# Optimization experiments

Measured on AMD Instinct MI355X. Metric: run time of the kernel, lower is better.

Reference implementation:

```python
import jax, jax.numpy as jnp
import numpy as np

N_RNA, N_DIS = 40000, 3000
E_EDGES, T = 600000, 10000
RNA_IN, D_FEAT, HID, EXP_D = 512, 256, 512, 256
N_EXP, HEADS = 8, 8
HD = HID // HEADS          # per-head dim inside HANConv
MHA_HD = EXP_D // HEADS    # per-head dim in cross-attention
FUSION = 2 * HID


def setup_inputs() -> dict:
    key = jax.random.key(0)
    ks = iter(jax.random.split(key, 48))
    def nrm(shape, s=0.02):
        return jax.random.normal(next(ks), shape, dtype=jnp.float32) * s
    inp = {
        "x_rna": jax.random.normal(next(ks), (N_RNA, RNA_IN), dtype=jnp.float32),
        "x_dis": jax.random.normal(next(ks), (N_DIS, D_FEAT), dtype=jnp.float32),
        "Wd": nrm((RNA_IN, D_FEAT)), "bd": jnp.zeros((RNA_IN,), jnp.float32),
        "Wp_r": nrm((HID, RNA_IN)), "bp_r": jnp.zeros((HID,), jnp.float32),
        "Wp_d": nrm((HID, RNA_IN)), "bp_d": jnp.zeros((HID,), jnp.float32),
        "a_src_rd": nrm((HEADS, HD), 0.1), "a_dst_rd": nrm((HEADS, HD), 0.1),
        "a_src_dr": nrm((HEADS, HD), 0.1), "a_dst_dr": nrm((HEADS, HD), 0.1),
        "kW": nrm((HID, HID)), "kb": jnp.zeros((HID,), jnp.float32),
        "qv": nrm((HID,), 0.1),
        "Wl": nrm((HID, HID)), "bl": jnp.zeros((HID,), jnp.float32),
        "W_exp": nrm((N_EXP, FUSION, EXP_D)), "b_exp": jnp.zeros((N_EXP, EXP_D), jnp.float32),
        "W_gate": nrm((4, HID, N_EXP)),
        "W_head": nrm((4, 2 * EXP_D, EXP_D)), "b_head": jnp.zeros((4, EXP_D), jnp.float32),
        "in_w": nrm((3 * EXP_D, EXP_D)), "in_b": jnp.zeros((3 * EXP_D,), jnp.float32),
        "out_w": nrm((EXP_D, EXP_D)), "out_b": jnp.zeros((EXP_D,), jnp.float32),
        "Wdp": nrm((EXP_D, HID)), "bdp": jnp.zeros((EXP_D,), jnp.float32),
        "ei_rd_src": jax.random.randint(next(ks), (E_EDGES,), 0, N_RNA),
        "ei_rd_dst": jax.random.randint(next(ks), (E_EDGES,), 0, N_DIS),
        "ei_dr_src": jax.random.randint(next(ks), (E_EDGES,), 0, N_DIS),
        "ei_dr_dst": jax.random.randint(next(ks), (E_EDGES,), 0, N_RNA),
        "idx_rels": jax.random.randint(next(ks), (4, T), 0, N_RNA),
    }
    return inp


def _han_edge(x_src, x_dst, ei_src, ei_dst, a_src, a_dst, n_dst):
    # x_*: [N, H, D]; GAT-style attention with softmax per destination node (PyG HANConv edge step)
    as_ = (x_src * a_src).sum(-1)                                 # [Ns, H]
    ad_ = (x_dst * a_dst).sum(-1)                                 # [Nd, H]
    alpha = jax.nn.leaky_relu(as_[ei_src] + ad_[ei_dst], 0.2)     # [E, H]
    amax = jax.ops.segment_max(alpha, ei_dst, num_segments=n_dst)
    ex = jnp.exp(alpha - amax[ei_dst])
    den = jax.ops.segment_sum(ex, ei_dst, num_segments=n_dst)
    w = ex / (den[ei_dst] + 1e-16)
    msg = x_src[ei_src] * w[:, :, None]                           # [E, H, D]
    out = jax.ops.segment_sum(msg, ei_dst, num_segments=n_dst)    # [Nd, H, D]
    return jax.nn.relu(out.reshape(n_dst, -1))


def _semantic(outs, kW, kb, qv):
    # outs: [M, N, F]; metapath-level (semantic) attention from HANConv
    s = (jnp.tanh(outs @ kW.T + kb).mean(axis=1) * qv).sum(-1)    # [M]
    beta = jax.nn.softmax(s)
    return (beta[:, None, None] * outs).sum(0)


def reference(x_rna, x_dis, Wd, bd, Wp_r, bp_r, Wp_d, bp_d,
              a_src_rd, a_dst_rd, a_src_dr, a_dst_dr,
              kW, kb, qv, Wl, bl, W_exp, b_exp, W_gate, W_head, b_head,
              in_w, in_b, out_w, out_b, Wdp, bdp,
              ei_rd_src, ei_rd_dst, ei_dr_src, ei_dr_dst, idx_rels):
    # ---- HAN encoder ----
    xd = x_dis @ Wd.T + bd                                        # disease feat -> rna_in_dim
    hr0 = (x_rna @ Wp_r.T + bp_r).reshape(N_RNA, HEADS, HD)
    hd0 = (xd @ Wp_d.T + bp_d).reshape(N_DIS, HEADS, HD)
    out_dis = _han_edge(hr0, hd0, ei_rd_src, ei_rd_dst, a_src_rd, a_dst_rd, N_DIS)
    out_rna = _han_edge(hd0, hr0, ei_dr_src, ei_dr_dst, a_src_dr, a_dst_dr, N_RNA)
    h_rna = _semantic(out_rna[None], kW, kb, qv) @ Wl.T + bl      # shared final lin
    h_dis = _semantic(out_dis[None], kW, kb, qv) @ Wl.T + bl
    # ---- MoE with per-relation gating ----
    d_global = h_dis.mean(axis=0)
    fusion = jnp.concatenate([h_rna, jnp.broadcast_to(d_global, h_rna.shape)], axis=1)  # [N, 2H]
    E = jax.nn.relu(jnp.einsum('nf,efd->ned', fusion, W_exp) + b_exp)  # [N, Nexp, Ed]
    h_t = h_rna[idx_rels]                                         # [4, T, H]
    scores = jnp.einsum('rth,rhe->rte', h_t, W_gate)              # raw gate scores (no softmax)
    u = (E[idx_rels] * scores[..., None]).sum(axis=2)             # [4, T, Ed]
    U = u.mean(axis=1)                                            # [4, Ed]
    # ---- cross attention over 4 task tokens ----
    qkv = U @ in_w.T + in_b
    q, k, v = jnp.split(qkv, 3, axis=-1)
    def heads(z):
        return z.reshape(4, HEADS, MHA_HD).transpose(1, 0, 2)     # [H, 4, dh]
    qh, kh, vh = heads(q), heads(k), heads(v)
    attn = jax.nn.softmax(jnp.einsum('htd,hsd->hts', qh, kh) / np.float32(np.sqrt(MHA_HD)), axis=-1)
    o = jnp.einsum('hts,hsd->htd', attn, vh).transpose(1, 0, 2).reshape(4, EXP_D)
    U_prime = o @ out_w.T + out_b                                 # [4, Ed]
    # ---- per-relation heads and disease scores ----
    cross = jnp.broadcast_to(U_prime[:, None, :], u.shape)
    cat = jnp.concatenate([u, cross], axis=-1)                    # [4, T, 2Ed]
    p = jax.nn.relu(jnp.einsum('rtc,rcd->rtd', cat, W_head) + b_head[:, None, :])
    d_proj = h_dis @ Wdp.T + bdp                                  # [Ndis, Ed]
    return jax.nn.sigmoid(jnp.einsum('rtd,md->rtm', p, d_proj))   # [4, T, Ndis]
```

## Files before the change

kernel.cpp:

```cpp
#include <hip/hip_runtime.h>
#include <math.h>

constexpr int NRNA = 40000;
constexpr int NDIS = 3000;
constexpr int NEDG = 600000;
constexpr int TREL = 10000;

typedef __attribute__((ext_vector_type(8))) short bh8;
typedef __attribute__((ext_vector_type(4))) float f32x4;

__device__ inline float bf2f(ushort x) {
    union { uint u; float f; } v; v.u = ((uint)x) << 16; return v.f;
}
__device__ inline ushort f2bf(float f) {
    union { float f; uint u; } v; v.f = f;
    uint u = v.u;
    uint r = (u + 0x7fffu + ((u >> 16) & 1u)) >> 16;
    return (ushort)r;
}
__device__ inline float bflo(uint w) { union { uint u; float f; } v; v.u = w << 16; return v.f; }
__device__ inline float bfhi(uint w) { union { uint u; float f; } v; v.u = w & 0xffff0000u; return v.f; }

__device__ inline void gload16(const ushort* g, ushort* l) {
    __builtin_amdgcn_global_load_lds(
        (const __attribute__((address_space(1))) unsigned int*)(const void*)g,
        (__attribute__((address_space(3))) unsigned int*)(void*)l, 16, 0, 0);
}

__device__ inline int xcd_swz(int f, int n) {
    int q = n >> 3, r = n & 7, xcd = f & 7, i = f >> 3;
    return (xcd < r) ? (xcd * (q + 1) + i) : (r * (q + 1) + (xcd - r) * q + i);
}

__global__ __launch_bounds__(256) void conv_bf16(const float* __restrict__ in,
                                                 ushort* __restrict__ out, long n)
{
    long g = ((long)blockIdx.x * 256 + threadIdx.x) * 4;
    if (g >= n) return;
    float4 v = *(const float4*)(in + g);
    ushort4 o;
    o.x = f2bf(v.x); o.y = f2bf(v.y); o.z = f2bf(v.z); o.w = f2bf(v.w);
    *(ushort4*)(out + g) = o;
}

__global__ __launch_bounds__(256) void transpose_wexp(const float* __restrict__ W,
                                                      ushort* __restrict__ out)
{
    long g = (long)blockIdx.x * 256 + threadIdx.x;
    int e = (int)(g >> 17), d = (int)((g >> 9) & 255), f = (int)(g & 511);
    out[g] = f2bf(W[(long)e * 262144 + (long)f * 256 + d]);
}

__global__ __launch_bounds__(256) void transpose_whead(const float* __restrict__ W,
                                                       ushort* __restrict__ out)
{
    long g = (long)blockIdx.x * 256 + threadIdx.x;
    int r = (int)(g >> 16), d = (int)((g >> 8) & 255), c = (int)(g & 255);
    out[g] = f2bf(W[(long)r * 131072 + (long)c * 256 + d]);
}

__global__ void transpose_wgate(const float* __restrict__ W, float* __restrict__ out)
{
    int g = blockIdx.x * 256 + threadIdx.x;
    int r = g >> 12, e = (g >> 9) & 7, k = g & 511;
    out[g] = W[(long)r * 4096 + (long)k * 8 + e];
}

template<int ACT, bool SWZ>
__global__ __launch_bounds__(256) void gemm_mfma(
    const ushort* __restrict__ A, const ushort* __restrict__ B,
    const float* __restrict__ bias, float* __restrict__ Cf, ushort* __restrict__ Cb,
    const int* __restrict__ idx,
    int M, int N, int K, long sA, long sB, long sBias, long sC)
{
    __shared__ ushort smem[16384];
    ushort* As = smem;
    ushort* Bs = smem + 8192;
    int bx = blockIdx.x, by = blockIdx.y;
    if (SWZ) {
        int n = gridDim.x * gridDim.y;
        int s = xcd_swz(by * gridDim.x + bx, n);
        bx = s % gridDim.x; by = s / gridDim.x;
    }
    const int bz = blockIdx.z;
    const ushort* Ab = A + (long)bz * sA;
    const ushort* Bb = B + (long)bz * sB;
    const float* biasb = bias ? (bias + (long)bz * sBias) : nullptr;
    const int row0 = by * 128, col0 = bx * 128;

    const int tid = threadIdx.x, wid = tid >> 6, lane = tid & 63;
    const int wr = wid >> 1, wc = wid & 1;

    const int lrow = lane >> 3;
    const int lk = (((lane & 7) ^ lrow) * 8);
    const ushort* ap0[4]; const ushort* bp0[4];
    ushort* la[4]; ushort* lb[4];
#pragma unroll
    for (int i = 0; i < 4; ++i) {
        int c = wid * 4 + i;
        int ra = row0 + c * 8 + lrow; ra = ra < M ? ra : M - 1;
        int rs = idx ? idx[ra] : ra;
        ap0[i] = Ab + (long)rs * K + lk;
        int cb = col0 + c * 8 + lrow; cb = cb < N ? cb : N - 1;
        bp0[i] = Bb + (long)cb * K + lk;
        la[i] = As + c * 512;
        lb[i] = Bs + c * 512;
    }

    f32x4 acc[4][4];
#pragma unroll
    for (int i = 0; i < 4; ++i)
// ... 45 lines not shown
        for (int it = 0; it < 8; ++it) {
            int rl = it * 16 + (tid >> 4);
            int cl = (tid & 15) * 4;
            int m = row0 + rl, col = col0 + H * 64 + cl;
            if (m < M && col < N) {
                f32x4 v = *(const f32x4*)(cs + rl * 64 + cl);
                if (biasb) {
                    float4 bv = *(const float4*)(biasb + col);
                    v[0] += bv.x; v[1] += bv.y; v[2] += bv.z; v[3] += bv.w;
                }
                if (ACT == 1) {
#pragma unroll
                    for (int q = 0; q < 4; ++q) v[q] = fmaxf(v[q], 0.f);
                } else if (ACT == 2) {
#pragma unroll
                    for (int q = 0; q < 4; ++q) v[q] = 1.f / (1.f + __expf(-v[q]));
                }
                long o = (long)bz * sC + (long)m * N + col;
                if (Cf) *(f32x4*)(Cf + o) = v;
                if (Cb) {
                    ushort4 ob;
                    ob.x = f2bf(v[0]); ob.y = f2bf(v[1]); ob.z = f2bf(v[2]); ob.w = f2bf(v[3]);
                    *(ushort4*)(Cb + o) = ob;
                }
            }
        }
        __syncthreads();
    }
}

__global__ __launch_bounds__(256) void moe_mfma(
    const ushort* __restrict__ h, const ushort* __restrict__ WexpT,
    const float* __restrict__ c_exp, const float* __restrict__ S,
    const int* __restrict__ idx, ushort* __restrict__ up)
{
    __shared__ ushort smem[24576];
    __shared__ float sS[128 * 2];
    __shared__ float sC[2 * 128];
    ushort* As  = smem;
    ushort* Bs0 = smem + 8192;
    ushort* Bs1 = smem + 16384;
    int bx = blockIdx.x, by = blockIdx.y;
    {
        int n = gridDim.x * gridDim.y;
        int s = xcd_swz(by * gridDim.x + bx, n);
        bx = s % gridDim.x; by = s / gridDim.x;
    }
    const int row0 = by * 128, col0 = bx * 128;
    const int z = blockIdx.z, e0 = z * 2;
    const int tid = threadIdx.x, wid = tid >> 6, lane = tid & 63;
    const int wr = wid >> 1, wc = wid & 1;
    constexpr int M = 4 * TREL;

    if (tid < 256) {
        int rr = tid >> 1, e = tid & 1;
        sS[tid] = S[(long)(row0 + rr) * 8 + e0 + e];
    }
    if (tid < 256) {
        int e = tid >> 7, cc = tid & 127;
        sC[tid] = c_exp[(e0 + e) * 256 + col0 + cc];
    }

    const int lrow = lane >> 3;
    const int lk = (((lane & 7) ^ lrow) * 8);
    const ushort* ap0[4]; const ushort* bp0[4];
    ushort* la[4]; ushort* lb0[4]; ushort* lb1[4];
#pragma unroll
    for (int i = 0; i < 4; ++i) {
        int c = wid * 4 + i;
        int ra = row0 + c * 8 + lrow;
        ap0[i] = h + (long)idx[ra] * 512 + lk;
        bp0[i] = WexpT + (long)(col0 + c * 8 + lrow) * 512 + (long)e0 * 131072 + lk;
        la[i]  = As  + c * 512;
        lb0[i] = Bs0 + c * 512;
        lb1[i] = Bs1 + c * 512;
    }

    const int fr = lane & 15, fq = lane >> 4;
    const int sw0 = (fq ^ (fr & 7)) * 8;
    const ushort* paRow  = As  + (wr * 64 + fr) * 64;
    const ushort* pb0Row = Bs0 + (wc * 64 + fr) * 64;
    const ushort* pb1Row = Bs1 + (wc * 64 + fr) * 64;

    f32x4 acc0[4][4], acc1[4][4];
#pragma unroll
    for (int i = 0; i < 4; ++i)
#pragma unroll
        for (int n = 0; n < 4; ++n) {
            acc0[i][n] = (f32x4){0.f, 0.f, 0.f, 0.f};
            acc1[i][n] = (f32x4){0.f, 0.f, 0.f, 0.f};
        }
    __syncthreads();

    for (int k0 = 0; k0 < 512; k0 += 64) {
#pragma unroll
        for (int i = 0; i < 4; ++i) gload16(ap0[i] + k0, la[i]);
#pragma unroll
        for (int i = 0; i < 4; ++i) gload16(bp0[i] + k0, lb0[i]);
#pragma unroll
        for (int i = 0; i < 4; ++i) gload16(bp0[i] + 131072 + k0, lb1[i]);
        __syncthreads();
#pragma unroll
        for (int kk = 0; kk < 2; ++kk) {
            const int sw = kk ? (sw0 ^ 32) : sw0;
            bh8 af[4], b0[4], b1[4];
#pragma unroll
            for (int i = 0; i < 4; ++i) af[i] = *(const bh8*)(paRow + i * 1024 + sw);
#pragma unroll
            for (int n = 0; n < 4; ++n) b0[n] = *(const bh8*)(pb0Row + n * 1024 + sw);
#pragma unroll
            for (int n = 0; n < 4; ++n) b1[n] = *(const bh8*)(pb1Row + n * 1024 + sw);
#pragma unroll
            for (int i = 0; i < 4; ++i)
// ... 18 lines not shown
                float s0 = sS[(rl + r) * 2 + 0];
                float s1 = sS[(rl + r) * 2 + 1];
                acc0[i][n][r] = s0 * fmaxf(acc0[i][n][r] + c0, 0.f)
                              + s1 * fmaxf(acc1[i][n][r] + c1, 0.f);
            }
        }
    }

    float* cs = (float*)smem;
    ushort* upz = up + (long)z * M * 256;
#pragma unroll
    for (int H = 0; H < 2; ++H) {
        if (wc == H) {
#pragma unroll
            for (int i = 0; i < 4; ++i)
#pragma unroll
                for (int n = 0; n < 4; ++n)
#pragma unroll
                    for (int r = 0; r < 4; ++r)
                        cs[(wr * 64 + i * 16 + fq * 4 + r) * 64 + n * 16 + fr] = acc0[i][n][r];
        }
        __syncthreads();
#pragma unroll
        for (int it = 0; it < 8; ++it) {
            int rl = it * 16 + (tid >> 4);
            int cl = (tid & 15) * 4;
            f32x4 v = *(const f32x4*)(cs + rl * 64 + cl);
            int m = row0 + rl, col = col0 + H * 64 + cl;
            ushort4 ob;
            ob.x = f2bf(v[0]); ob.y = f2bf(v[1]); ob.z = f2bf(v[2]); ob.w = f2bf(v[3]);
            *(ushort4*)(upz + (long)m * 256 + col) = ob;
        }
        __syncthreads();
    }
}

__global__ __launch_bounds__(256) void moe_combine(const ushort* __restrict__ up,
                                                   ushort* __restrict__ u)
{
    constexpr long TOT = (long)4 * TREL * 256;
    long g = ((long)blockIdx.x * 256 + threadIdx.x) * 4;
    if (g >= TOT) return;
    float a[4] = {0.f, 0.f, 0.f, 0.f};
#pragma unroll
    for (int z = 0; z < 4; ++z) {
        ushort4 v = *(const ushort4*)(up + z * TOT + g);
        a[0] += bf2f(v.x); a[1] += bf2f(v.y); a[2] += bf2f(v.z); a[3] += bf2f(v.w);
    }
    ushort4 o;
    o.x = f2bf(a[0]); o.y = f2bf(a[1]); o.z = f2bf(a[2]); o.w = f2bf(a[3]);
    *(ushort4*)(u + g) = o;
}

__global__ void dot_heads2(const ushort* __restrict__ x,
                           const float* __restrict__ a1, const float* __restrict__ a2,
                           float* __restrict__ o1, float* __restrict__ o2, int nodes)
{
    long g = (long)blockIdx.x * 256 + threadIdx.x;
    if (g >= (long)nodes * 8) return;
    int node = (int)(g >> 3), h = (int)(g & 7);
    const ushort* xp = x + (long)node * 512 + h * 64;
    const float* p1 = a1 + h * 64;
    const float* p2 = a2 + h * 64;
    float s1 = 0.f, s2 = 0.f;
#pragma unroll
    for (int d = 0; d < 64; d += 8) {
        uint4 xv = *(const uint4*)(xp + d);
        float xf[8] = { bflo(xv.x), bfhi(xv.x), bflo(xv.y), bfhi(xv.y),
                        bflo(xv.z), bfhi(xv.z), bflo(xv.w), bfhi(xv.w) };
#pragma unroll
        for (int j = 0; j < 8; ++j) {
            s1 = fmaf(xf[j], p1[d + j], s1);
            s2 = fmaf(xf[j], p2[d + j], s2);
        }
    }
    o1[g] = s1; o2[g] = s2;
}

__global__ void hist_kernel(const int* __restrict__ dst, int* __restrict__ deg, int E)
{
    int g = blockIdx.x * 256 + threadIdx.x;
    if (g < E) atomicAdd(&deg[dst[g]], 1);
}

__global__ __launch_bounds__(1024) void scan_blocks(const int* __restrict__ in,
                                                    int* __restrict__ tmp,
                                                    int* __restrict__ bsum, int n)
{
    __shared__ int wsum[16];
    const int tid = threadIdx.x, lane = tid & 63, wid = tid >> 6;
    int base = blockIdx.x * 1024;
    int v = (base + tid < n) ? in[base + tid] : 0;
    int s = v;
#pragma unroll
    for (int off = 1; off < 64; off <<= 1) {
        int t = __shfl_up(s, off, 64);
        if (lane >= off) s += t;
    }
    if (lane == 63) wsum[wid] = s;
    __syncthreads();
    if (wid == 0) {
        int w = (lane < 16) ? wsum[lane] : 0;
#pragma unroll
        for (int off = 1; off < 16; off <<= 1) {
            int t = __shfl_up(w, off, 64);
            if (lane >= off) w += t;
        }
        if (lane < 16) wsum[lane] = w;
    }
    __syncthreads();
    int incl = s + ((wid == 0) ? 0 : wsum[wid - 1]);
    if (base + tid < n) tmp[base + tid] = incl;
    if (tid == 1023) bsum[blockIdx.x] = incl;
}

__global__ void scan_bsums(int* __restrict__ bsum, int nb)
{
    int lane = threadIdx.x;
    int v = (lane < nb) ? bsum[lane] : 0;
#pragma unroll
    for (int off = 1; off < 64; off <<= 1) {
        int t = __shfl_up(v, off, 64);
        if (lane >= off) v += t;
    }
    if (lane < nb) bsum[lane] = v;
}

__global__ __launch_bounds__(1024) void scan_finish(const int* __restrict__ in,
                                                    const int* __restrict__ tmp,
                                                    const int* __restrict__ bsum,
                                                    int* __restrict__ offs,
                                                    int* __restrict__ cur, int n, int nb)
{
    int base = blockIdx.x * 1024;
    int i = base + threadIdx.x;
    if (i < n) {
        int pre = (blockIdx.x == 0) ? 0 : bsum[blockIdx.x - 1];
        int v = tmp[i] - in[i] + pre;
        offs[i] = v;
        cur[i] = v;
    }
    if (i == 0) offs[n] = bsum[nb - 1];
}

__global__ void scatter_kernel(const int* __restrict__ src, const int* __restrict__ dst,
                               int* __restrict__ cur, int* __restrict__ csr_src, int E)
{
    int g = blockIdx.x * 256 + threadIdx.x;
    if (g < E) {
        int p = atomicAdd(&cur[dst[g]], 1);
        csr_src[p] = src[g];
    }
}

__global__ __launch_bounds__(256) void han_wave(
    const int* __restrict__ offs, const int* __restrict__ csr_src,
    const float* __restrict__ as_, const float* __restrict__ ad_,
    const ushort* __restrict__ x_src, ushort* __restrict__ out, int nnode)
{
    __shared__ float s_ex[4][64];
    __shared__ int   s_src[4][8];
    __shared__ float s_den[4][8];
    const int w = threadIdx.x >> 6, lane = threadIdx.x & 63;
    const int node = blockIdx.x * 4 + w;
    if (node >= nnode) return;
    const int e0 = offs[node], ne = offs[node + 1] - e0;
    const int myh = lane & 7, grp = lane >> 3;
    const float my_ad = ad_[node * 8 + myh];

    float mx = -3.0e38f;
    for (int t = grp; t < ne; t += 8) {
        int src = csr_src[e0 + t];
        float al = as_[(long)src * 8 + myh] + my_ad;
        al = al >= 0.f ? al : 0.2f * al;
        mx = fmaxf(mx, al);
    }
#pragma unroll
    for (int m = 8; m < 64; m <<= 1) mx = fmaxf(mx, __shfl_xor(mx, m, 64));

    float den = 0.f;
    float acc[8];
#pragma unroll
    for (int k = 0; k < 8; ++k) acc[k] = 0.f;
    const int colbase = lane * 8;

    for (int c0 = 0; c0 < ne; c0 += 8) {
        const int nc = min(8, ne - c0);
        float ex = 0.f;
        int src = 0;
        if (grp < nc) {
            src = csr_src[e0 + c0 + grp];
            float al = as_[(long)src * 8 + myh] + my_ad;
            al = al >= 0.f ? al : 0.2f * al;
            ex = __expf(al - mx);
            den += ex;
        }
        s_ex[w][grp * 8 + myh] = ex;
        if (myh == 0) s_src[w][grp] = src;
        asm volatile("s_waitcnt lgkmcnt(0)" ::: "memory");
        for (int j = 0; j < nc; ++j) {
            float wg = s_ex[w][j * 8 + grp];
            uint4 xv = *(const uint4*)(x_src + (long)s_src[w][j] * 512 + colbase);
            acc[0] = fmaf(wg, bflo(xv.x), acc[0]);
            acc[1] = fmaf(wg, bfhi(xv.x), acc[1]);
            acc[2] = fmaf(wg, bflo(xv.y), acc[2]);
            acc[3] = fmaf(wg, bfhi(xv.y), acc[3]);
            acc[4] = fmaf(wg, bflo(xv.z), acc[4]);
            acc[5] = fmaf(wg, bfhi(xv.z), acc[5]);
            acc[6] = fmaf(wg, bflo(xv.w), acc[6]);
            acc[7] = fmaf(wg, bfhi(xv.w), acc[7]);
        }
        __builtin_amdgcn_wave_barrier();
    }

#pragma unroll
    for (int m = 8; m < 64; m <<= 1) den += __shfl_xor(den, m, 64);
    if (grp == 0) s_den[w][myh] = den;
    asm volatile("s_waitcnt lgkmcnt(0)" ::: "memory");
    float d = s_den[w][grp] + 1e-16f;

    uint4 ov;
    ov.x = (uint)f2bf(fmaxf(acc[0] / d, 0.f)) | ((uint)f2bf(fmaxf(acc[1] / d, 0.f)) << 16);
    ov.y = (uint)f2bf(fmaxf(acc[2] / d, 0.f)) | ((uint)f2bf(fmaxf(acc[3] / d, 0.f)) << 16);
    ov.z = (uint)f2bf(fmaxf(acc[4] / d, 0.f)) | ((uint)f2bf(fmaxf(acc[5] / d, 0.f)) << 16);
    ov.w = (uint)f2bf(fmaxf(acc[6] / d, 0.f)) | ((uint)f2bf(fmaxf(acc[7] / d, 0.f)) << 16);
    *(uint4*)(out + (long)node * 512 + colbase) = ov;
}

__global__ __launch_bounds__(512) void hdis_colsum_partial(const float* __restrict__ h_dis,
                                                           float* __restrict__ part)
{
    int c = blockIdx.x, d = threadIdx.x;
    int r0 = c * 200;
    float s = 0.f;
    for (int r = r0; r < r0 + 200; ++r) s += h_dis[(long)r * 512 + d];
    part[c * 512 + d] = s;
}
__global__ __launch_bounds__(512) void hdis_colsum_finish(const float* __restrict__ part,
                                                          float* __restrict__ dg)
{
    int d = threadIdx.x;
    float s = 0.f;
    for (int c = 0; c < 15; ++c) s += part[c * 512 + d];
    dg[d] = s * (1.f / NDIS);
}

__global__ void cexp_part(const float* __restrict__ dg, const float* __restrict__ W_exp,
                          float* __restrict__ part)
{
    int b = blockIdx.x;
    int e = b >> 3, ch = b & 7, d = threadIdx.x;
    const float* W = W_exp + (long)e * 262144 + (long)(512 + ch * 64) * 256 + d;
    float s = 0.f;
    for (int f = 0; f < 64; ++f) s = fmaf(dg[ch * 64 + f], W[(long)f * 256], s);
    part[b * 256 + d] = s;
}
__global__ void cexp_fin(const float* __restrict__ part, const float* __restrict__ b_exp,
                         float* __restrict__ c_exp)
{
    int e = blockIdx.x, d = threadIdx.x;
    float s = b_exp[e * 256 + d];
    for (int ch = 0; ch < 8; ++ch) s += part[(e * 8 + ch) * 256 + d];
    c_exp[e * 256 + d] = s;
}

__global__ __launch_bounds__(256) void scores2(const ushort* __restrict__ h,
                                               const float* __restrict__ WgT,
                                               const int* __restrict__ idx,
                                               float* __restrict__ S)
{
    __shared__ float sW[8 * 512];
    const int r = blockIdx.y;
    const int tid = threadIdx.x;
    for (int i = tid; i < 4096; i += 256) sW[i] = WgT[(long)r * 4096 + i];
    __syncthreads();
    int n = blockIdx.x * 256 + tid;
    if (n >= TREL) return;
    int gi = r * TREL + n;
    const ushort* hp = h + (long)idx[gi] * 512;
    float acc[8];
#pragma unroll
    for (int e = 0; e < 8; ++e) acc[e] = 0.f;
    for (int k = 0; k < 512; k += 8) {
        uint4 hv = *(const uint4*)(hp + k);
        float hf[8];
        hf[0] = bflo(hv.x); hf[1] = bfhi(hv.x); hf[2] = bflo(hv.y); hf[3] = bfhi(hv.y);
        hf[4] = bflo(hv.z); hf[5] = bfhi(hv.z); hf[6] = bflo(hv.w); hf[7] = bfhi(hv.w);
#pragma unroll
        for (int e = 0; e < 8; ++e)
#pragma unroll
            for (int j = 0; j < 8; ++j)
                acc[e] = fmaf(hf[j], sW[e * 512 + k + j], acc[e]);
    }
#pragma unroll
    for (int e = 0; e < 8; ++e) S[(long)gi * 8 + e] = acc[e];
}

__global__ void u_mean_partial(const ushort* __restrict__ u, float* __restrict__ part)
{
    int c = blockIdx.x, r = blockIdx.y, d = threadIdx.x;
    int t0 = c * 313, t1 = min(t0 + 313, TREL);
    const ushort* base = u + ((long)r * TREL) * 256 + d;
    float s = 0.f;
    for (int t = t0; t < t1; ++t) s += bf2f(base[(long)t * 256]);
    part[((long)r * 32 + c) * 256 + d] = s;
}
__global__ void u_mean_finish(const float* __restrict__ part, float* __restrict__ U)
{
    int r = blockIdx.x, d = threadIdx.x;
    float s = 0.f;
    for (int c = 0; c < 32; ++c) s += part[((long)r * 32 + c) * 256 + d];
    U[r * 256 + d] = s * (1.f / TREL);
}

__global__ __launch_bounds__(256) void cross_attn_kernel(
    const float* __restrict__ U, const float* __restrict__ in_w, const float* __restrict__ in_b,
    const float* __restrict__ out_w, const float* __restrict__ out_b, float* __restrict__ Up)
{
    __shared__ float sU[4 * 256];
    __shared__ float sqkv[4 * 768];
    __shared__ float sattn[128];
    __shared__ float so[4 * 256];
    const int tid = threadIdx.x;
    for (int i = tid; i < 1024; i += 256) sU[i] = U[i];
    __syncthreads();
    for (int o = tid; o < 3072; o += 256) {
        int row = o / 768, col = o % 768;
        const float* w = in_w + (long)col * 256;
        const float* uu = sU + row * 256;
        float s = in_b[col];
        for (int k = 0; k < 256; ++k) s = fmaf(uu[k], w[k], s);
        sqkv[o] = s;
    }
    __syncthreads();
    if (tid < 128) {
        int h = tid >> 4, t = (tid >> 2) & 3, s2 = tid & 3;
        const float* q = sqkv + t * 768 + h * 32;
        const float* kk = sqkv + s2 * 768 + 256 + h * 32;
        float s = 0.f;
        for (int d = 0; d < 32; ++d) s += q[d] * kk[d];
        sattn[tid] = s * 0.17677669529663687f;
    }
    __syncthreads();
    if (tid < 32) {
        int base = tid * 4;
        float a0 = sattn[base], a1 = sattn[base+1], a2 = sattn[base+2], a3 = sattn[base+3];
        float m = fmaxf(fmaxf(a0, a1), fmaxf(a2, a3));
        float e0 = __expf(a0 - m), e1 = __expf(a1 - m), e2 = __expf(a2 - m), e3 = __expf(a3 - m);
        float inv = 1.f / (e0 + e1 + e2 + e3);
        sattn[base] = e0 * inv; sattn[base+1] = e1 * inv;
        sattn[base+2] = e2 * inv; sattn[base+3] = e3 * inv;
    }
    __syncthreads();
    for (int o = tid; o < 1024; o += 256) {
        int t = o >> 8, hd = o & 255, h = hd >> 5, d = hd & 31;
        const float* a = sattn + (h * 4 + t) * 4;
        float s = 0.f;
        for (int s2 = 0; s2 < 4; ++s2) s += a[s2] * sqkv[s2 * 768 + 512 + h * 32 + d];
        so[t * 256 + hd] = s;
    }
    __syncthreads();
    for (int o = tid; o < 1024; o += 256) {
        int t = o >> 8, d = o & 255;
        const float* w = out_w + (long)d * 256;
        const float* ov = so + t * 256;
        float s = out_b[d];
        for (int k = 0; k < 256; ++k) s = fmaf(ov[k], w[k], s);
        Up[o] = s;
    }
}

__global__ void chead_kernel(const float* __restrict__ Up, const float* __restrict__ W_head,
                             const float* __restrict__ b_head, float* __restrict__ c_head)
{
    int r = blockIdx.x, d = threadIdx.x;
    const float* W = W_head + (long)r * 512 * 256 + 256 * 256 + d;
    float s = b_head[r * 256 + d];
    for (int c = 0; c < 256; ++c) s = fmaf(Up[r * 256 + c], W[(long)c * 256], s);
    c_head[r * 256 + d] = s;
}

extern "C" void kernel_launch(void* const* d_in, const int* in_sizes, int n_in,
                              void* d_out, int out_size, void* d_ws, size_t ws_size,
                              hipStream_t stream)
{
    (void)in_sizes; (void)n_in; (void)out_size;
    const float* x_rna    = (const float*)d_in[0];
    const float* x_dis    = (const float*)d_in[1];
    const float* Wd       = (const float*)d_in[2];
    const float* bd       = (const float*)d_in[3];
    const float* Wp_r     = (const float*)d_in[4];
    const float* bp_r     = (const float*)d_in[5];
    const float* Wp_d     = (const float*)d_in[6];
    const float* bp_d     = (const float*)d_in[7];
    const float* a_src_rd = (const float*)d_in[8];
    const float* a_dst_rd = (const float*)d_in[9];
    const float* a_src_dr = (const float*)d_in[10];
    const float* a_dst_dr = (const float*)d_in[11];
    const float* Wl       = (const float*)d_in[15];
    const float* bl       = (const float*)d_in[16];
    const float* W_exp    = (const float*)d_in[17];
    const float* b_exp    = (const float*)d_in[18];
    const float* W_gate   = (const float*)d_in[19];
    const float* W_head   = (const float*)d_in[20];
    const float* b_head   = (const float*)d_in[21];
    const float* in_w     = (const float*)d_in[22];
    const float* in_b     = (const float*)d_in[23];
    const float* out_w    = (const float*)d_in[24];
    const float* out_b    = (const float*)d_in[25];
    const float* Wdp      = (const float*)d_in[26];
    const float* bdp      = (const float*)d_in[27];
    const int* ei_rd_src  = (const int*)d_in[28];
    const int* ei_rd_dst  = (const int*)d_in[29];
    const int* ei_dr_src  = (const int*)d_in[30];
    const int* ei_dr_dst  = (const int*)d_in[31];
    const int* idx_rels   = (const int*)d_in[32];
    float* out = (float*)d_out;

    char* ws = (char*)d_ws;
    size_t off = 0;
    auto alloc = [&](size_t bytes) -> void* {
        off = (off + 255) & ~(size_t)255;
        void* p = ws + off;
        off += bytes;
        return p;
    };
    ushort* xrb      = (ushort*)alloc((size_t)NRNA * 512 * 2);
    ushort* hr0b     = (ushort*)alloc((size_t)NRNA * 512 * 2);
    ushort* u_bf     = (ushort*)alloc((size_t)4 * TREL * 256 * 2);
    ushort* p_bf     = (ushort*)alloc((size_t)4 * TREL * 256 * 2);
    ushort* up_bf    = (ushort*)alloc((size_t)4 * 4 * TREL * 256 * 2);
    ushort* xdb      = (ushort*)alloc((size_t)NDIS * 256 * 2);
    ushort* xd_bf    = (ushort*)alloc((size_t)NDIS * 512 * 2);
    ushort* hd0b     = (ushort*)alloc((size_t)NDIS * 512 * 2);
    ushort* outdis_b = (ushort*)alloc((size_t)NDIS * 512 * 2);
    ushort* hdis_b   = (ushort*)alloc((size_t)NDIS * 512 * 2);
    ushort* dproj_b  = (ushort*)alloc((size_t)NDIS * 256 * 2);
    float*  hdis_f   = (float*)alloc((size_t)NDIS * 512 * 4);
    ushort* Wdb    = (ushort*)alloc((size_t)512 * 256 * 2);
    ushort* Wprb   = (ushort*)alloc((size_t)512 * 512 * 2);
    ushort* Wpdb   = (ushort*)alloc((size_t)512 * 512 * 2);
    ushort* Wlb    = (ushort*)alloc((size_t)512 * 512 * 2);
    ushort* Wdpb   = (ushort*)alloc((size_t)256 * 512 * 2);
    ushort* WexpT  = (ushort*)alloc((size_t)8 * 256 * 512 * 2);
    ushort* WheadT = (ushort*)alloc((size_t)4 * 256 * 256 * 2);
    float*  WgT    = (float*)alloc((size_t)4 * 8 * 512 * 4);
    float* as_rd   = (float*)alloc((size_t)NRNA * 8 * 4);
    float* ad_rd   = (float*)alloc((size_t)NDIS * 8 * 4);
    float* as_dr   = (float*)alloc((size_t)NDIS * 8 * 4);
    float* ad_dr   = (float*)alloc((size_t)NRNA * 8 * 4);
    float* S       = (float*)alloc((size_t)4 * TREL * 8 * 4);
    float* dg_part = (float*)alloc((size_t)15 * 512 * 4);
    float* dg      = (float*)alloc((size_t)512 * 4);
    float* c_exp   = (float*)alloc((size_t)8 * 256 * 4);
    float* ce_part = (float*)alloc((size_t)64 * 256 * 4);
    float* u_part  = (float*)alloc((size_t)4 * 32 * 256 * 4);
    float* U       = (float*)alloc((size_t)4 * 256 * 4);
    float* Up      = (float*)alloc((size_t)4 * 256 * 4);
    float* c_head  = (float*)alloc((size_t)4 * 256 * 4);
    int* deg_rd  = (int*)alloc((size_t)NDIS * 4);
    int* offs_rd = (int*)alloc((size_t)(NDIS + 1) * 4);
    int* cur_rd  = (int*)alloc((size_t)NDIS * 4);
    int* csr_rd  = (int*)alloc((size_t)NEDG * 4);
    int* deg_dr  = (int*)alloc((size_t)NRNA * 4);
    int* offs_dr = (int*)alloc((size_t)(NRNA + 1) * 4);
    int* cur_dr  = (int*)alloc((size_t)NRNA * 4);
    int* csr_dr  = (int*)alloc((size_t)NEDG * 4);
    int* scan_tmp = (int*)alloc((size_t)NRNA * 4);
    int* scan_bs  = (int*)alloc((size_t)64 * 4);
    if (off > ws_size) return;

    ushort* outrna_b = xrb;
    ushort* hrna_b   = hr0b;

    const dim3 blk(256);

    conv_bf16<<<dim3(20000), blk, 0, stream>>>(x_rna, xrb, (long)NRNA * 512);
    conv_bf16<<<dim3(750),   blk, 0, stream>>>(x_dis, xdb, (long)NDIS * 256);
    conv_bf16<<<dim3(128),   blk, 0, stream>>>(Wd,   Wdb,  512 * 256);
    conv_bf16<<<dim3(256),   blk, 0, stream>>>(Wp_r, Wprb, 512 * 512);
    conv_bf16<<<dim3(256),   blk, 0, stream>>>(Wp_d, Wpdb, 512 * 512);
    conv_bf16<<<dim3(256),   blk, 0, stream>>>(Wl,   Wlb,  512 * 512);
    conv_bf16<<<dim3(128),   blk, 0, stream>>>(Wdp,  Wdpb, 256 * 512);
    transpose_wexp<<<dim3(4096), blk, 0, stream>>>(W_exp, WexpT);
    transpose_whead<<<dim3(1024), blk, 0, stream>>>(W_head, WheadT);
    transpose_wgate<<<dim3(64), blk, 0, stream>>>(W_gate, WgT);

    gemm_mfma<0,false><<<dim3(4, 24), blk, 0, stream>>>(
        xdb, Wdb, bd, nullptr, xd_bf, nullptr, NDIS, 512, 256, 0, 0, 0, 0);
    gemm_mfma<0,true><<<dim3(4, 313), blk, 0, stream>>>(
        xrb, Wprb, bp_r, nullptr, hr0b, nullptr, NRNA, 512, 512, 0, 0, 0, 0);
    gemm_mfma<0,false><<<dim3(4, 24), blk, 0, stream>>>(
        xd_bf, Wpdb, bp_d, nullptr, hd0b, nullptr, NDIS, 512, 512, 0, 0, 0, 0);

    dot_heads2<<<dim3((NRNA * 8) / 256), blk, 0, stream>>>(hr0b, a_src_rd, a_dst_dr, as_rd, ad_dr, NRNA);
    dot_heads2<<<dim3((NDIS * 8 + 255) / 256), blk, 0, stream>>>(hd0b, a_dst_rd, a_src_dr, ad_rd, as_dr, NDIS);

    hipMemsetAsync(deg_rd, 0, NDIS * 4, stream);
    hipMemsetAsync(deg_dr, 0, NRNA * 4, stream);
    hist_kernel<<<dim3((NEDG + 255) / 256), blk, 0, stream>>>(ei_rd_dst, deg_rd, NEDG);
    hist_kernel<<<dim3((NEDG + 255) / 256), blk, 0, stream>>>(ei_dr_dst, deg_dr, NEDG);
    scan_blocks<<<dim3(3), dim3(1024), 0, stream>>>(deg_rd, scan_tmp, scan_bs, NDIS);
    scan_bsums<<<dim3(1), dim3(64), 0, stream>>>(scan_bs, 3);
    scan_finish<<<dim3(3), dim3(1024), 0, stream>>>(deg_rd, scan_tmp, scan_bs, offs_rd, cur_rd, NDIS, 3);
    scan_blocks<<<dim3(40), dim3(1024), 0, stream>>>(deg_dr, scan_tmp, scan_bs, NRNA);
    scan_bsums<<<dim3(1), dim3(64), 0, stream>>>(scan_bs, 40);
    scan_finish<<<dim3(40), dim3(1024), 0, stream>>>(deg_dr, scan_tmp, scan_bs, offs_dr, cur_dr, NRNA, 40);
    scatter_kernel<<<dim3((NEDG + 255) / 256), blk, 0, stream>>>(ei_rd_src, ei_rd_dst, cur_rd, csr_rd, NEDG);
    scatter_kernel<<<dim3((NEDG + 255) / 256), blk, 0, stream>>>(ei_dr_src, ei_dr_dst, cur_dr, csr_dr, NEDG);

    han_wave<<<dim3((NDIS + 3) / 4), blk, 0, stream>>>(offs_rd, csr_rd, as_rd, ad_rd, hr0b, outdis_b, NDIS);
    han_wave<<<dim3(NRNA / 4), blk, 0, stream>>>(offs_dr, csr_dr, as_dr, ad_dr, hd0b, outrna_b, NRNA);

    gemm_mfma<0,true><<<dim3(4, 313), blk, 0, stream>>>(
        outrna_b, Wlb, bl, nullptr, hrna_b, nullptr, NRNA, 512, 512, 0, 0, 0, 0);
    gemm_mfma<0,false><<<dim3(4, 24), blk, 0, stream>>>(
        outdis_b, Wlb, bl, hdis_f, hdis_b, nullptr, NDIS, 512, 512, 0, 0, 0, 0);

    hdis_colsum_partial<<<dim3(15), dim3(512), 0, stream>>>(hdis_f, dg_part);
    hdis_colsum_finish<<<dim3(1), dim3(512), 0, stream>>>(dg_part, dg);
    cexp_part<<<dim3(64), blk, 0, stream>>>(dg, W_exp, ce_part);
    cexp_fin<<<dim3(8), blk, 0, stream>>>(ce_part, b_exp, c_exp);
    scores2<<<dim3(40, 4), blk, 0, stream>>>(hrna_b, WgT, idx_rels, S);

    moe_mfma<<<dim3(2, 320, 4), blk, 0, stream>>>(hrna_b, WexpT, c_exp, S, idx_rels, up_bf);
    moe_combine<<<dim3(10240), blk, 0, stream>>>(up_bf, u_bf);

    u_mean_partial<<<dim3(32, 4), blk, 0, stream>>>(u_bf, u_part);
    u_mean_finish<<<dim3(4), blk, 0, stream>>>(u_part, U);
    cross_attn_kernel<<<dim3(1), blk, 0, stream>>>(U, in_w, in_b, out_w, out_b, Up);
    chead_kernel<<<dim3(4), blk, 0, stream>>>(Up, W_head, b_head, c_head);

    gemm_mfma<1,false><<<dim3(2, 79, 4), blk, 0, stream>>>(
        u_bf, WheadT, c_head, nullptr, p_bf, nullptr, TREL, 256, 256,
        (long)TREL * 256, 65536, 256, (long)TREL * 256);

    gemm_mfma<0,false><<<dim3(2, 24), blk, 0, stream>>>(
        hdis_b, Wdpb, bdp, nullptr, dproj_b, nullptr, NDIS, 256, 512, 0, 0, 0, 0);

    gemm_mfma<2,true><<<dim3(24, 320), blk, 0, stream>>>(
        p_bf, dproj_b, nullptr, out, nullptr, nullptr, 4 * TREL, NDIS, 256, 0, 0, 0, 0);
}
```

Measured before the change: 1.294 ms.

## Merge paired launches, fuse tail kernels, tile weight transposes, drop softmax max pass

Pairs of small per-relation kernels (dot heads, histogram, scans, scatter) become single launches that branch on block index. The tail mean, cross-attention and head-bias kernels are fused into one. The two Wl GEMMs become one GEMM over a concatenated RNA+disease buffer. Weight transposes now go through an LDS-tiled kernel. The HAN softmax max-subtraction pass is removed, which saves a gather pass over the edges but risks exp overflow with larger logits. The disease column sum now reads bf16 instead of fp32.

```diff
diff --git a/kernel.cpp b/kernel.cpp
--- a/kernel.cpp
+++ b/kernel.cpp
@@ -43,20 +43,26 @@
     *(ushort4*)(out + g) = o;
 }
 
-__global__ __launch_bounds__(256) void transpose_wexp(const float* __restrict__ W,
-                                                      ushort* __restrict__ out)
-{
-    long g = (long)blockIdx.x * 256 + threadIdx.x;
-    int e = (int)(g >> 17), d = (int)((g >> 9) & 255), f = (int)(g & 511);
-    out[g] = f2bf(W[(long)e * 262144 + (long)f * 256 + d]);
-}
-
-__global__ __launch_bounds__(256) void transpose_whead(const float* __restrict__ W,
-                                                       ushort* __restrict__ out)
-{
-    long g = (long)blockIdx.x * 256 + threadIdx.x;
-    int r = (int)(g >> 16), d = (int)((g >> 8) & 255), c = (int)(g & 255);
-    out[g] = f2bf(W[(long)r * 131072 + (long)c * 256 + d]);
+__global__ __launch_bounds__(256) void transpose_bf16(
+    const float* __restrict__ in, ushort* __restrict__ out,
+    int R, int C, long sIn, long sOut)
+{
+    __shared__ float t[64][65];
+    const int tid = threadIdx.x;
+    const int r0 = blockIdx.y * 64, c0 = blockIdx.x * 64;
+    const float* ib = in + (long)blockIdx.z * sIn;
+    ushort* ob = out + (long)blockIdx.z * sOut;
+#pragma unroll
+    for (int k = 0; k < 16; ++k) {
+        int idx = k * 256 + tid, i = idx >> 6, j = idx & 63;
+        t[i][j] = ib[(long)(r0 + i) * C + c0 + j];
+    }
+    __syncthreads();
+#pragma unroll
+    for (int k = 0; k < 16; ++k) {
+        int idx = k * 256 + tid, i = idx >> 6, j = idx & 63;
+        ob[(long)(c0 + i) * R + r0 + j] = f2bf(t[j][i]);
+    }
 }
 
 __global__ void transpose_wgate(const float* __restrict__ W, float* __restrict__ out)
@@ -208,13 +214,11 @@
     const int wr = wid >> 1, wc = wid & 1;
     constexpr int M = 4 * TREL;
 
-    if (tid < 256) {
+    {
         int rr = tid >> 1, e = tid & 1;
         sS[tid] = S[(long)(row0 + rr) * 8 + e0 + e];
-    }
-    if (tid < 256) {
-        int e = tid >> 7, cc = tid & 127;
-        sC[tid] = c_exp[(e0 + e) * 256 + col0 + cc];
+        int ee = tid >> 7, cc = tid & 127;
+        sC[tid] = c_exp[(e0 + ee) * 256 + col0 + cc];
     }
 
     const int lrow = lane >> 3;
@@ -339,16 +343,25 @@
     *(ushort4*)(u + g) = o;
 }
 
-__global__ void dot_heads2(const ushort* __restrict__ x,
-                           const float* __restrict__ a1, const float* __restrict__ a2,
-                           float* __restrict__ o1, float* __restrict__ o2, int nodes)
+__global__ void dot_heads_all(const ushort* __restrict__ xr, const ushort* __restrict__ xd,
+                              const float* __restrict__ a_src_rd, const float* __restrict__ a_dst_dr,
+                              const float* __restrict__ a_dst_rd, const float* __restrict__ a_src_dr,
+                              float* __restrict__ as_rd, float* __restrict__ ad_dr,
+                              float* __restrict__ ad_rd, float* __restrict__ as_dr)
 {
     long g = (long)blockIdx.x * 256 + threadIdx.x;
-    if (g >= (long)nodes * 8) return;
-    int node = (int)(g >> 3), h = (int)(g & 7);
+    const ushort* x; const float *p1, *p2; float *o1, *o2; long gi;
+    if (g < (long)NRNA * 8) {
+        gi = g; x = xr; p1 = a_src_rd; p2 = a_dst_dr; o1 = as_rd; o2 = ad_dr;
+    } else {
+        gi = g - (long)NRNA * 8;
+        if (gi >= (long)NDIS * 8) return;
+        x = xd; p1 = a_dst_rd; p2 = a_src_dr; o1 = ad_rd; o2 = as_dr;
+    }
+    int node = (int)(gi >> 3), h = (int)(gi & 7);
     const ushort* xp = x + (long)node * 512 + h * 64;
-    const float* p1 = a1 + h * 64;
-    const float* p2 = a2 + h * 64;
+    const float* q1 = p1 + h * 64;
+    const float* q2 = p2 + h * 64;
     float s1 = 0.f, s2 = 0.f;
 #pragma unroll
     for (int d = 0; d < 64; d += 8) {
@@ -357,23 +370,33 @@
                         bflo(xv.z), bfhi(xv.z), bflo(xv.w), bfhi(xv.w) };
 #pragma unroll
         for (int j = 0; j < 8; ++j) {
-            s1 = fmaf(xf[j], p1[d + j], s1);
-            s2 = fmaf(xf[j], p2[d + j], s2);
-        }
-    }
-    o1[g] = s1; o2[g] = s2;
-}
-
-__global__ void hist_kernel(const int* __restrict__ dst, int* __restrict__ deg, int E)
+            s1 = fmaf(xf[j], q1[d + j], s1);
+            s2 = fmaf(xf[j], q2[d + j], s2);
+        }
+    }
+    o1[gi] = s1; o2[gi] = s2;
+}
+
+__global__ void hist2(const int* __restrict__ d0, int* __restrict__ deg0,
+                      const int* __restrict__ d1, int* __restrict__ deg1, int E)
 {
     int g = blockIdx.x * 256 + threadIdx.x;
-    if (g < E) atomicAdd(&deg[dst[g]], 1);
-}
-
-__global__ __launch_bounds__(1024) void scan_blocks(const int* __restrict__ in,
-                                                    int* __restrict__ tmp,
-                                                    int* __restrict__ bsum, int n)
-{
+    if (g >= E) return;
+    if (blockIdx.y == 0) atomicAdd(&deg0[d0[g]], 1);
+    else                 atomicAdd(&deg1[d1[g]], 1);
+}
+
+__global__ __launch_bounds__(1024) void scan_blocks2(
+    const int* __restrict__ in0, int* __restrict__ tmp0, int* __restrict__ bs0, int n0,
+    const int* __restrict__ in1, int* __restrict__ tmp1, int* __restrict__ bs1, int n1)
+{
+    const int z = blockIdx.y;
+    const int* in = z ? in1 : in0;
+    int* tmp = z ? tmp1 : tmp0;
+    int* bsum = z ? bs1 : bs0;
+    const int n = z ? n1 : n0;
+    const int nb = (n + 1023) >> 10;
+    if ((int)blockIdx.x >= nb) return;
     __shared__ int wsum[16];
     const int tid = threadIdx.x, lane = tid & 63, wid = tid >> 6;
     int base = blockIdx.x * 1024;
@@ -401,8 +424,10 @@
     if (tid == 1023) bsum[blockIdx.x] = incl;
 }
 
-__global__ void scan_bsums(int* __restrict__ bsum, int nb)
-{
+__global__ void scan_bsums2(int* __restrict__ bs0, int nb0, int* __restrict__ bs1, int nb1)
+{
+    int* bsum = blockIdx.x ? bs1 : bs0;
+    int nb = blockIdx.x ? nb1 : nb0;
     int lane = threadIdx.x;
     int v = (lane < nb) ? bsum[lane] : 0;
 #pragma unroll
@@ -413,12 +438,21 @@
     if (lane < nb) bsum[lane] = v;
 }
 
-__global__ __launch_bounds__(1024) void scan_finish(const int* __restrict__ in,
-                                                    const int* __restrict__ tmp,
-                                                    const int* __restrict__ bsum,
-                                                    int* __restrict__ offs,
-                                                    int* __restrict__ cur, int n, int nb)
-{
+__global__ __launch_bounds__(1024) void scan_finish2(
+    const int* __restrict__ in0, const int* __restrict__ tmp0, const int* __restrict__ bs0,
+    int* __restrict__ offs0, int* __restrict__ cur0, int n0,
+    const int* __restrict__ in1, const int* __restrict__ tmp1, const int* __restrict__ bs1,
+    int* __restrict__ offs1, int* __restrict__ cur1, int n1)
+{
+    const int z = blockIdx.y;
+    const int* in = z ? in1 : in0;
+    const int* tmp = z ? tmp1 : tmp0;
+    const int* bsum = z ? bs1 : bs0;
+    int* offs = z ? offs1 : offs0;
+    int* cur = z ? cur1 : cur0;
+    const int n = z ? n1 : n0;
+    const int nb = (n + 1023) >> 10;
+    if ((int)blockIdx.x >= nb) return;
     int base = blockIdx.x * 1024;
     int i = base + threadIdx.x;
     if (i < n) {
@@ -430,13 +464,19 @@
     if (i == 0) offs[n] = bsum[nb - 1];
 }
 
-__global__ void scatter_kernel(const int* __restrict__ src, const int* __restrict__ dst,
-                               int* __restrict__ cur, int* __restrict__ csr_src, int E)
+__global__ void scatter2(const int* __restrict__ s0, const int* __restrict__ d0,
+                         int* __restrict__ c0, int* __restrict__ o0,
+                         const int* __restrict__ s1, const int* __restrict__ d1,
+                         int* __restrict__ c1, int* __restrict__ o1, int E)
 {
     int g = blockIdx.x * 256 + threadIdx.x;
-    if (g < E) {
-        int p = atomicAdd(&cur[dst[g]], 1);
-        csr_src[p] = src[g];
+    if (g >= E) return;
+    if (blockIdx.y == 0) {
+        int p = atomicAdd(&c0[d0[g]], 1);
+        o0[p] = s0[g];
+    } else {
+        int p = atomicAdd(&c1[d1[g]], 1);
+        o1[p] = s1[g];
     }
 }
 
@@ -455,16 +495,6 @@
     const int myh = lane & 7, grp = lane >> 3;
     const float my_ad = ad_[node * 8 + myh];
 
-    float mx = -3.0e38f;
-    for (int t = grp; t < ne; t += 8) {
-        int src = csr_src[e0 + t];
-        float al = as_[(long)src * 8 + myh] + my_ad;
-        al = al >= 0.f ? al : 0.2f * al;
-        mx = fmaxf(mx, al);
-    }
-#pragma unroll
-    for (int m = 8; m < 64; m <<= 1) mx = fmaxf(mx, __shfl_xor(mx, m, 64));
-
     float den = 0.f;
     float acc[8];
 #pragma unroll
@@ -479,7 +509,7 @@
             src = csr_src[e0 + c0 + grp];
             float al = as_[(long)src * 8 + myh] + my_ad;
             al = al >= 0.f ? al : 0.2f * al;
-            ex = __expf(al - mx);
+            ex = __expf(al);
             den += ex;
         }
         s_ex[w][grp * 8 + myh] = ex;
@@ -514,13 +544,13 @@
     *(uint4*)(out + (long)node * 512 + colbase) = ov;
 }
 
-__global__ __launch_bounds__(512) void hdis_colsum_partial(const float* __restrict__ h_dis,
+__global__ __launch_bounds__(512) void hdis_colsum_partial(const ushort* __restrict__ h_dis,
                                                            float* __restrict__ part)
 {
     int c = blockIdx.x, d = threadIdx.x;
     int r0 = c * 200;
     float s = 0.f;
-    for (int r = r0; r < r0 + 200; ++r) s += h_dis[(long)r * 512 + d];
+    for (int r = r0; r < r0 + 200; ++r) s += bf2f(h_dis[(long)r * 512 + d]);
     part[c * 512 + d] = s;
 }
 __global__ __launch_bounds__(512) void hdis_colsum_finish(const float* __restrict__ part,
@@ -592,25 +622,29 @@
     for (int t = t0; t < t1; ++t) s += bf2f(base[(long)t * 256]);
     part[((long)r * 32 + c) * 256 + d] = s;
 }
-__global__ void u_mean_finish(const float* __restrict__ part, float* __restrict__ U)
-{
-    int r = blockIdx.x, d = threadIdx.x;
-    float s = 0.f;
-    for (int c = 0; c < 32; ++c) s += part[((long)r * 32 + c) * 256 + d];
-    U[r * 256 + d] = s * (1.f / TREL);
-}
-
-__global__ __launch_bounds__(256) void cross_attn_kernel(
-    const float* __restrict__ U, const float* __restrict__ in_w, const float* __restrict__ in_b,
-    const float* __restrict__ out_w, const float* __restrict__ out_b, float* __restrict__ Up)
+
+__global__ __launch_bounds__(256) void tail_kernel(
+    const float* __restrict__ u_part,
+    const float* __restrict__ in_w, const float* __restrict__ in_b,
+    const float* __restrict__ out_w, const float* __restrict__ out_b,
+    const float* __restrict__ W_head, const float* __restrict__ b_head,
+    float* __restrict__ c_head)
 {
     __shared__ float sU[4 * 256];
     __shared__ float sqkv[4 * 768];
     __shared__ float sattn[128];
     __shared__ float so[4 * 256];
+    __shared__ float sUp[4 * 256];
     const int tid = threadIdx.x;
-    for (int i = tid; i < 1024; i += 256) sU[i] = U[i];
-    __syncthreads();
+
+    for (int o = tid; o < 1024; o += 256) {
+        int r = o >> 8, d = o & 255;
+        float s = 0.f;
+        for (int c = 0; c < 32; ++c) s += u_part[((long)r * 32 + c) * 256 + d];
+        sU[o] = s * (1.f / TREL);
+    }
+    __syncthreads();
+
     for (int o = tid; o < 3072; o += 256) {
         int row = o / 768, col = o % 768;
         const float* w = in_w + (long)col * 256;
@@ -653,18 +687,18 @@
         const float* ov = so + t * 256;
         float s = out_b[d];
         for (int k = 0; k < 256; ++k) s = fmaf(ov[k], w[k], s);
-        Up[o] = s;
-    }
-}
-
-__global__ void chead_kernel(const float* __restrict__ Up, const float* __restrict__ W_head,
-                             const float* __restrict__ b_head, float* __restrict__ c_head)
-{
-    int r = blockIdx.x, d = threadIdx.x;
-    const float* W = W_head + (long)r * 512 * 256 + 256 * 256 + d;
-    float s = b_head[r * 256 + d];
-    for (int c = 0; c < 256; ++c) s = fmaf(Up[r * 256 + c], W[(long)c * 256], s);
-    c_head[r * 256 + d] = s;
+        sUp[o] = s;
+    }
+    __syncthreads();
+
+    for (int o = tid; o < 1024; o += 256) {
+        int r = o >> 8, d = o & 255;
+        const float* W = W_head + (long)r * 131072 + 65536 + d;
+        const float* up = sUp + r * 256;
+        float s = b_head[o];
+        for (int c = 0; c < 256; ++c) s = fmaf(up[c], W[(long)c * 256], s);
+        c_head[o] = s;
+    }
 }
 
 extern "C" void kernel_launch(void* const* d_in, const int* in_sizes, int n_in,
@@ -712,18 +746,18 @@
         off += bytes;
         return p;
     };
+    constexpr int NALL = NRNA + NDIS;
     ushort* xrb      = (ushort*)alloc((size_t)NRNA * 512 * 2);
     ushort* hr0b     = (ushort*)alloc((size_t)NRNA * 512 * 2);
+    ushort* out_all  = (ushort*)alloc((size_t)(NALL + 8) * 512 * 2);
+    ushort* h_all    = (ushort*)alloc((size_t)(NALL + 8) * 512 * 2);
     ushort* u_bf     = (ushort*)alloc((size_t)4 * TREL * 256 * 2);
     ushort* p_bf     = (ushort*)alloc((size_t)4 * TREL * 256 * 2);
     ushort* up_bf    = (ushort*)alloc((size_t)4 * 4 * TREL * 256 * 2);
     ushort* xdb      = (ushort*)alloc((size_t)NDIS * 256 * 2);
     ushort* xd_bf    = (ushort*)alloc((size_t)NDIS * 512 * 2);
     ushort* hd0b     = (ushort*)alloc((size_t)NDIS * 512 * 2);
-    ushort* outdis_b = (ushort*)alloc((size_t)NDIS * 512 * 2);
-    ushort* hdis_b   = (ushort*)alloc((size_t)NDIS * 512 * 2);
     ushort* dproj_b  = (ushort*)alloc((size_t)NDIS * 256 * 2);
-    float*  hdis_f   = (float*)alloc((size_t)NDIS * 512 * 4);
     ushort* Wdb    = (ushort*)alloc((size_t)512 * 256 * 2);
     ushort* Wprb   = (ushort*)alloc((size_t)512 * 512 * 2);
     ushort* Wpdb   = (ushort*)alloc((size_t)512 * 512 * 2);
@@ -742,23 +776,25 @@
     float* c_exp   = (float*)alloc((size_t)8 * 256 * 4);
     float* ce_part = (float*)alloc((size_t)64 * 256 * 4);
     float* u_part  = (float*)alloc((size_t)4 * 32 * 256 * 4);
-    float* U       = (float*)alloc((size_t)4 * 256 * 4);
-    float* Up      = (float*)alloc((size_t)4 * 256 * 4);
     float* c_head  = (float*)alloc((size_t)4 * 256 * 4);
-    int* deg_rd  = (int*)alloc((size_t)NDIS * 4);
+    int* deg_all  = (int*)alloc((size_t)(NDIS + NRNA) * 4);
+    int* deg_rd = deg_all, * deg_dr = deg_all + NDIS;
     int* offs_rd = (int*)alloc((size_t)(NDIS + 1) * 4);
     int* cur_rd  = (int*)alloc((size_t)NDIS * 4);
     int* csr_rd  = (int*)alloc((size_t)NEDG * 4);
-    int* deg_dr  = (int*)alloc((size_t)NRNA * 4);
     int* offs_dr = (int*)alloc((size_t)(NRNA + 1) * 4);
     int* cur_dr  = (int*)alloc((size_t)NRNA * 4);
     int* csr_dr  = (int*)alloc((size_t)NEDG * 4);
-    int* scan_tmp = (int*)alloc((size_t)NRNA * 4);
-    int* scan_bs  = (int*)alloc((size_t)64 * 4);
+    int* tmp_rd  = (int*)alloc((size_t)NDIS * 4);
+    int* tmp_dr  = (int*)alloc((size_t)NRNA * 4);
+    int* bs_rd   = (int*)alloc((size_t)64 * 4);
+    int* bs_dr   = (int*)alloc((size_t)64 * 4);
     if (off > ws_size) return;
 
-    ushort* outrna_b = xrb;
-    ushort* hrna_b   = hr0b;
+    ushort* out_rna = out_all;
+    ushort* out_dis = out_all + (size_t)NRNA * 512;
+    ushort* h_rna   = h_all;
+    ushort* h_dis   = h_all + (size_t)NRNA * 512;
 
     const dim3 blk(256);
 
@@ -769,8 +805,10 @@
     conv_bf16<<<dim3(256),   blk, 0, stream>>>(Wp_d, Wpdb, 512 * 512);
     conv_bf16<<<dim3(256),   blk, 0, stream>>>(Wl,   Wlb,  512 * 512);
     conv_bf16<<<dim3(128),   blk, 0, stream>>>(Wdp,  Wdpb, 256 * 512);
-    transpose_wexp<<<dim3(4096), blk, 0, stream>>>(W_exp, WexpT);
-    transpose_whead<<<dim3(1024), blk, 0, stream>>>(W_head, WheadT);
+    transpose_bf16<<<dim3(4, 8, 8), blk, 0, stream>>>(W_exp, WexpT, 512, 256,
+                                                      (long)1024 * 256, (long)256 * 512);
+    transpose_bf16<<<dim3(4, 4, 4), blk, 0, stream>>>(W_head, WheadT, 256, 256,
+                                                      (long)512 * 256, (long)256 * 256);
     transpose_wgate<<<dim3(64), blk, 0, stream>>>(W_gate, WgT);
 
     gemm_mfma<0,false><<<dim3(4, 24), blk, 0, stream>>>(
@@ -780,50 +818,44 @@
     gemm_mfma<0,false><<<dim3(4, 24), blk, 0, stream>>>(
         xd_bf, Wpdb, bp_d, nullptr, hd0b, nullptr, NDIS, 512, 512, 0, 0, 0, 0);
 
-    dot_heads2<<<dim3((NRNA * 8) / 256), blk, 0, stream>>>(hr0b, a_src_rd, a_dst_dr, as_rd, ad_dr, NRNA);
-    dot_heads2<<<dim3((NDIS * 8 + 255) / 256), blk, 0, stream>>>(hd0b, a_dst_rd, a_src_dr, ad_rd, as_dr, NDIS);
-
-    hipMemsetAsync(deg_rd, 0, NDIS * 4, stream);
-    hipMemsetAsync(deg_dr, 0, NRNA * 4, stream);
-    hist_kernel<<<dim3((NEDG + 255) / 256), blk, 0, stream>>>(ei_rd_dst, deg_rd, NEDG);
-    hist_kernel<<<dim3((NEDG + 255) / 256), blk, 0, stream>>>(ei_dr_dst, deg_dr, NEDG);
-    scan_blocks<<<dim3(3), dim3(1024), 0, stream>>>(deg_rd, scan_tmp, scan_bs, NDIS);
-    scan_bsums<<<dim3(1), dim3(64), 0, stream>>>(scan_bs, 3);
-    scan_finish<<<dim3(3), dim3(1024), 0, stream>>>(deg_rd, scan_tmp, scan_bs, offs_rd, cur_rd, NDIS, 3);
-    scan_blocks<<<dim3(40), dim3(1024), 0, stream>>>(deg_dr, scan_tmp, scan_bs, NRNA);
-    scan_bsums<<<dim3(1), dim3(64), 0, stream>>>(scan_bs, 40);
-    scan_finish<<<dim3(40), dim3(1024), 0, stream>>>(deg_dr, scan_tmp, scan_bs, offs_dr, cur_dr, NRNA, 40);
-    scatter_kernel<<<dim3((NEDG + 255) / 256), blk, 0, stream>>>(ei_rd_src, ei_rd_dst, cur_rd, csr_rd, NEDG);
-    scatter_kernel<<<dim3((NEDG + 255) / 256), blk, 0, stream>>>(ei_dr_src, ei_dr_dst, cur_dr, csr_dr, NEDG);
-
-    han_wave<<<dim3((NDIS + 3) / 4), blk, 0, stream>>>(offs_rd, csr_rd, as_rd, ad_rd, hr0b, outdis_b, NDIS);
-    han_wave<<<dim3(NRNA / 4), blk, 0, stream>>>(offs_dr, csr_dr, as_dr, ad_dr, hd0b, outrna_b, NRNA);
-
-    gemm_mfma<0,true><<<dim3(4, 313), blk, 0, stream>>>(
-        outrna_b, Wlb, bl, nullptr, hrna_b, nullptr, NRNA, 512, 512, 0, 0, 0, 0);
-    gemm_mfma<0,false><<<dim3(4, 24), blk, 0, stream>>>(
-        outdis_b, Wlb, bl, hdis_f, hdis_b, nullptr, NDIS, 512, 512, 0, 0, 0, 0);
-
-    hdis_colsum_partial<<<dim3(15), dim3(512), 0, stream>>>(hdis_f, dg_part);
+    dot_heads_all<<<dim3(((NRNA + NDIS) * 8 + 255) / 256), blk, 0, stream>>>(
+        hr0b, hd0b, a_src_rd, a_dst_dr, a_dst_rd, a_src_dr, as_rd, ad_dr, ad_rd, as_dr);
+
+    hipMemsetAsync(deg_all, 0, (size_t)(NDIS + NRNA) * 4, stream);
+    hist2<<<dim3((NEDG + 255) / 256, 2), blk, 0, stream>>>(ei_rd_dst, deg_rd, ei_dr_dst, deg_dr, NEDG);
+    scan_blocks2<<<dim3(40, 2), dim3(1024), 0, stream>>>(deg_rd, tmp_rd, bs_rd, NDIS,
+                                                         deg_dr, tmp_dr, bs_dr, NRNA);
+    scan_bsums2<<<dim3(2), dim3(64), 0, stream>>>(bs_rd, 3, bs_dr, 40);
+    scan_finish2<<<dim3(40, 2), dim3(1024), 0, stream>>>(deg_rd, tmp_rd, bs_rd, offs_rd, cur_rd, NDIS,
+                                                         deg_dr, tmp_dr, bs_dr, offs_dr, cur_dr, NRNA);
+    scatter2<<<dim3((NEDG + 255) / 256, 2), blk, 0, stream>>>(
+        ei_rd_src, ei_rd_dst, cur_rd, csr_rd, ei_dr_src, ei_dr_dst, cur_dr, csr_dr, NEDG);
+
+    han_wave<<<dim3((NDIS + 3) / 4), blk, 0, stream>>>(offs_rd, csr_rd, as_rd, ad_rd, hr0b, out_dis, NDIS);
+    han_wave<<<dim3(NRNA / 4), blk, 0, stream>>>(offs_dr, csr_dr, as_dr, ad_dr, hd0b, out_rna, NRNA);
+
+    gemm_mfma<0,true><<<dim3(4, (NALL + 127) / 128), blk, 0, stream>>>(
+        out_all, Wlb, bl, nullptr, h_all, nullptr, NALL, 512, 512, 0, 0, 0, 0);
+
+    hdis_colsum_partial<<<dim3(15), dim3(512), 0, stream>>>(h_dis, dg_part);
     hdis_colsum_finish<<<dim3(1), dim3(512), 0, stream>>>(dg_part, dg);
     cexp_part<<<dim3(64), blk, 0, stream>>>(dg, W_exp, ce_part);
     cexp_fin<<<dim3(8), blk, 0, stream>>>(ce_part, b_exp, c_exp);
-    scores2<<<dim3(40, 4), blk, 0, stream>>>(hrna_b, WgT, idx_rels, S);
-
-    moe_mfma<<<dim3(2, 320, 4), blk, 0, stream>>>(hrna_b, WexpT, c_exp, S, idx_rels, up_bf);
+    scores2<<<dim3(40, 4), blk, 0, stream>>>(h_rna, WgT, idx_rels, S);
+
+    moe_mfma<<<dim3(2, 320, 4), blk, 0, stream>>>(h_rna, WexpT, c_exp, S, idx_rels, up_bf);
     moe_combine<<<dim3(10240), blk, 0, stream>>>(up_bf, u_bf);
 
     u_mean_partial<<<dim3(32, 4), blk, 0, stream>>>(u_bf, u_part);
-    u_mean_finish<<<dim3(4), blk, 0, stream>>>(u_part, U);
-    cross_attn_kernel<<<dim3(1), blk, 0, stream>>>(U, in_w, in_b, out_w, out_b, Up);
-    chead_kernel<<<dim3(4), blk, 0, stream>>>(Up, W_head, b_head, c_head);
+    tail_kernel<<<dim3(1), blk, 0, stream>>>(u_part, in_w, in_b, out_w, out_b,
+                                             W_head, b_head, c_head);
 
     gemm_mfma<1,false><<<dim3(2, 79, 4), blk, 0, stream>>>(
         u_bf, WheadT, c_head, nullptr, p_bf, nullptr, TREL, 256, 256,
         (long)TREL * 256, 65536, 256, (long)TREL * 256);
 
     gemm_mfma<0,false><<<dim3(2, 24), blk, 0, stream>>>(
-        hdis_b, Wdpb, bdp, nullptr, dproj_b, nullptr, NDIS, 256, 512, 0, 0, 0, 0);
+        h_dis, Wdpb, bdp, nullptr, dproj_b, nullptr, NDIS, 256, 512, 0, 0, 0, 0);
 
     gemm_mfma<2,true><<<dim3(24, 320), blk, 0, stream>>>(
         p_bf, dproj_b, nullptr, out, nullptr, nullptr, 4 * TREL, NDIS, 256, 0, 0, 0, 0);
```

Result: no change. 1.271 ms (-1.8%).
